# Kernel optimization log

Hardware: AMD Instinct MI355X
Metric: run time of the kernel (lower is better)

Reference implementation:

```python
import jax, jax.numpy as jnp
import numpy as np

B, C, F, H = 262144, 16, 16, 12   # batch, n_clusters, cluster_size, ceil(0.75*F)
HH = 12                           # head hidden = ceil(0.75*C)
EPS = 1e-16


def _linear_init(key, shape, fan_in):
    # torch nn.Linear default: U(-1/sqrt(fan_in), 1/sqrt(fan_in))
    bound = 1.0 / np.sqrt(fan_in)
    return jax.random.uniform(key, shape, jnp.float32, -bound, bound)


def setup_inputs() -> dict:
    key = jax.random.key(0)
    ks = jax.random.split(key, 9)
    x = jax.random.normal(ks[0], (B, C * F), dtype=jnp.float32)
    cluster_idx = jnp.arange(C * F, dtype=jnp.int32).reshape(C, F)
    # Tail autoencoders, stacked over clusters (torch Linear layout [out,in])
    We = _linear_init(ks[1], (C, H, F), F)   # encoder weight per cluster
    be = _linear_init(ks[2], (C, H), F)      # encoder bias
    Wd = _linear_init(ks[3], (C, F, H), H)   # decoder weight per cluster
    bd = _linear_init(ks[4], (C, F), H)      # decoder bias
    # Head autoencoder
    He = _linear_init(ks[5], (HH, C), C)
    hbe = _linear_init(ks[6], (HH,), C)
    Hd = _linear_init(ks[7], (C, HH), HH)
    hbd = _linear_init(ks[8], (C,), HH)
    return {"x": x, "We": We, "be": be, "Wd": Wd, "bd": bd,
            "He": He, "hbe": hbe, "Hd": Hd, "hbd": hbd,
            "cluster_idx": cluster_idx}


def reference(x, We, be, Wd, bd, He, hbe, Hd, hbd, cluster_idx):
    # Gather per-cluster features: [B, C, F]
    xc = x[:, cluster_idx]
    # Normalization with default norm params (min=0, max=1)
    xc = (xc - 0.0) / (1.0 - 0.0 + EPS)
    # Grouped tail autoencoders: sigmoid(Linear) twice, batched over clusters
    h = jax.nn.sigmoid(jnp.einsum('bcf,chf->bch', xc, We) + be)
    rec = jax.nn.sigmoid(jnp.einsum('bch,cfh->bcf', h, Wd) + bd)
    # Per-cluster RMSE over batch and features -> [C]
    loss = jnp.sqrt(jnp.mean((rec - xc) ** 2, axis=(0, 2)))
    loss = jnp.where(loss == 0.0, jnp.float32(0.01), loss)
    # Output normalization (min=0, max=1)
    tails = (loss - 0.0) / (1.0 - 0.0 + EPS)
    # Head autoencoder on the 1-D tail-loss vector
    h2 = jax.nn.sigmoid(He @ tails + hbe)
    head_out = jax.nn.sigmoid(Hd @ h2 + hbd)
    return head_out, tails
```

## Files before the change

### kernel.cpp

```cpp
#include <hip/hip_runtime.h>
#include <math.h>

#define NB      262144
#define NC      16
#define NF      16
#define NH      12
#define NHH     12
#define THREADS 256
#define BX      (NB / THREADS)

__device__ __forceinline__ float sigmoid_fast(float z) {
    float e = __expf(-z);
    return __builtin_amdgcn_rcpf(1.0f + e);
}

__global__ __launch_bounds__(THREADS) void ae_main(
    const float* __restrict__ x,
    const float* __restrict__ We,
    const float* __restrict__ be,
    const float* __restrict__ Wd,
    const float* __restrict__ bd,
    float* __restrict__ partials)
{
    const int tid  = threadIdx.x;
    const int lane = tid & 63;
    const int wave = tid >> 6;
    const size_t b = (size_t)blockIdx.x * THREADS + tid;

    __shared__ float wred[NC][4];

    const float4* xp = reinterpret_cast<const float4*>(x + b * (NC * NF));

    float4 b0 = xp[0], b1 = xp[1], b2 = xp[2], b3 = xp[3];

    #pragma unroll 1
    for (int c = 0; c < NC; ++c) {
        float xc[NF];
        xc[0]=b0.x;  xc[1]=b0.y;  xc[2]=b0.z;  xc[3]=b0.w;
        xc[4]=b1.x;  xc[5]=b1.y;  xc[6]=b1.z;  xc[7]=b1.w;
        xc[8]=b2.x;  xc[9]=b2.y;  xc[10]=b2.z; xc[11]=b2.w;
        xc[12]=b3.x; xc[13]=b3.y; xc[14]=b3.z; xc[15]=b3.w;

        const int cn = (c + 1 < NC) ? (c + 1) : c;
        b0 = xp[4*cn+0]; b1 = xp[4*cn+1]; b2 = xp[4*cn+2]; b3 = xp[4*cn+3];

        const float* wec = We + c * (NH * NF);
        const float* bec = be + c * NH;
        float h[NH];
        #pragma unroll
        for (int hh = 0; hh < NH; ++hh) {
            float z = bec[hh];
            #pragma unroll
            for (int f = 0; f < NF; ++f)
                z = fmaf(xc[f], wec[hh * NF + f], z);
            h[hh] = sigmoid_fast(z);
        }

        const float* wdc = Wd + c * (NF * NH);
        const float* bdc = bd + c * NF;
        float lsum = 0.0f;
        #pragma unroll
        for (int f = 0; f < NF; ++f) {
            float z = bdc[f];
            #pragma unroll
            for (int hh = 0; hh < NH; ++hh)
                z = fmaf(h[hh], wdc[f * NH + hh], z);
            float r = sigmoid_fast(z);
            float d = r - xc[f];
            lsum = fmaf(d, d, lsum);
        }

        #pragma unroll
        for (int off = 32; off > 0; off >>= 1)
            lsum += __shfl_down(lsum, off, 64);
        if (lane == 0) wred[c][wave] = lsum;
    }

    __syncthreads();
    if (tid < NC) {
        float s = wred[tid][0] + wred[tid][1] + wred[tid][2] + wred[tid][3];
        partials[(size_t)blockIdx.x * NC + tid] = s;
    }
}

__global__ __launch_bounds__(1024) void ae_final(
    const float* __restrict__ partials,
    const float* __restrict__ He,
    const float* __restrict__ hbe,
    const float* __restrict__ Hd,
    const float* __restrict__ hbd,
    float* __restrict__ out)
{
    __shared__ float red[NC][65];
    __shared__ float tails_s[NC];
    __shared__ float h2_s[NHH];

    const int tid = threadIdx.x;
    const int c = tid & 15;
    const int g = tid >> 4;

    float s = 0.0f;
    for (int bx = g; bx < BX; bx += 64)
        s += partials[(size_t)bx * NC + c];
    red[c][g] = s;
    __syncthreads();

    if (tid < NC) {
        float t = 0.0f;
        #pragma unroll
        for (int g2 = 0; g2 < 64; ++g2) t += red[tid][g2];
        float loss = sqrtf(t * (1.0f / 4194304.0f));
        if (loss == 0.0f) loss = 0.01f;
        tails_s[tid] = loss;
        out[16 + tid] = loss;
    }
    __syncthreads();

    if (tid < NHH) {
        float z = hbe[tid];
        #pragma unroll
        for (int cc = 0; cc < NC; ++cc)
            z = fmaf(He[tid * NC + cc], tails_s[cc], z);
        h2_s[tid] = 1.0f / (1.0f + __expf(-z));
    }
    __syncthreads();

    if (tid < NC) {
        float z = hbd[tid];
        #pragma unroll
        for (int j = 0; j < NHH; ++j)
            z = fmaf(Hd[tid * NHH + j], h2_s[j], z);
        out[tid] = 1.0f / (1.0f + __expf(-z));
    }
}

extern "C" void kernel_launch(void* const* d_in, const int* in_sizes, int n_in,
                              void* d_out, int out_size, void* d_ws, size_t ws_size,
                              hipStream_t stream) {
    const float* x   = (const float*)d_in[0];
    const float* We  = (const float*)d_in[1];
    const float* be  = (const float*)d_in[2];
    const float* Wd  = (const float*)d_in[3];
    const float* bd  = (const float*)d_in[4];
    const float* He  = (const float*)d_in[5];
    const float* hbe = (const float*)d_in[6];
    const float* Hd  = (const float*)d_in[7];
    const float* hbd = (const float*)d_in[8];

    float* out      = (float*)d_out;
    float* partials = (float*)d_ws;

    ae_main<<<BX, THREADS, 0, stream>>>(x, We, be, Wd, bd, partials);
    ae_final<<<1, 1024, 0, stream>>>(partials, He, hbe, Hd, hbd, out);
}
```

Measured before the change: 452.7 us.

## Split clusters across grid y so each block handles two clusters

The main kernel's grid now has a second dimension over cluster pairs, so each block processes two clusters with all x loads issued up front instead of looping over all 16 with a one-step prefetch. This multiplies the block count by eight to expose more parallelism and memory-level concurrency. The partials layout and the final reduction are reindexed to match. In exchange, each thread's row reads are now strided 128-byte chunks rather than one contiguous 1 KB row, and there are more blocks to schedule.

```diff
diff --git a/kernel.cpp b/kernel.cpp
--- a/kernel.cpp
+++ b/kernel.cpp
@@ -8,6 +8,8 @@
 #define NHH     12
 #define THREADS 256
 #define BX      (NB / THREADS)
+#define NPAIR   8
+#define CPP     2
 
 __device__ __forceinline__ float sigmoid_fast(float z) {
     float e = __expf(-z);
@@ -25,25 +27,28 @@
     const int tid  = threadIdx.x;
     const int lane = tid & 63;
     const int wave = tid >> 6;
+    const int c0   = blockIdx.y * CPP;
     const size_t b = (size_t)blockIdx.x * THREADS + tid;
 
-    __shared__ float wred[NC][4];
+    __shared__ float wred[CPP][4];
 
-    const float4* xp = reinterpret_cast<const float4*>(x + b * (NC * NF));
+    const float4* xp = reinterpret_cast<const float4*>(
+        x + b * (NC * NF) + (size_t)c0 * NF);
 
-    float4 b0 = xp[0], b1 = xp[1], b2 = xp[2], b3 = xp[3];
+    float4 v[2 * 4];
+    #pragma unroll
+    for (int k = 0; k < 8; ++k) v[k] = xp[k];
 
-    #pragma unroll 1
-    for (int c = 0; c < NC; ++c) {
+    #pragma unroll
+    for (int j = 0; j < CPP; ++j) {
         float xc[NF];
-        xc[0]=b0.x;  xc[1]=b0.y;  xc[2]=b0.z;  xc[3]=b0.w;
-        xc[4]=b1.x;  xc[5]=b1.y;  xc[6]=b1.z;  xc[7]=b1.w;
-        xc[8]=b2.x;  xc[9]=b2.y;  xc[10]=b2.z; xc[11]=b2.w;
-        xc[12]=b3.x; xc[13]=b3.y; xc[14]=b3.z; xc[15]=b3.w;
+        #pragma unroll
+        for (int k = 0; k < 4; ++k) {
+            xc[4*k+0] = v[4*j+k].x; xc[4*k+1] = v[4*j+k].y;
+            xc[4*k+2] = v[4*j+k].z; xc[4*k+3] = v[4*j+k].w;
+        }
 
-        const int cn = (c + 1 < NC) ? (c + 1) : c;
-        b0 = xp[4*cn+0]; b1 = xp[4*cn+1]; b2 = xp[4*cn+2]; b3 = xp[4*cn+3];
-
+        const int c = c0 + j;
         const float* wec = We + c * (NH * NF);
         const float* bec = be + c * NH;
         float h[NH];
@@ -73,13 +78,13 @@
         #pragma unroll
         for (int off = 32; off > 0; off >>= 1)
             lsum += __shfl_down(lsum, off, 64);
-        if (lane == 0) wred[c][wave] = lsum;
+        if (lane == 0) wred[j][wave] = lsum;
     }
 
     __syncthreads();
-    if (tid < NC) {
+    if (tid < CPP) {
         float s = wred[tid][0] + wred[tid][1] + wred[tid][2] + wred[tid][3];
-        partials[(size_t)blockIdx.x * NC + tid] = s;
+        partials[((size_t)blockIdx.y * BX + blockIdx.x) * CPP + tid] = s;
     }
 }
 
@@ -98,10 +103,11 @@
     const int tid = threadIdx.x;
     const int c = tid & 15;
     const int g = tid >> 4;
+    const int py = c >> 1, jj = c & 1;
 
     float s = 0.0f;
     for (int bx = g; bx < BX; bx += 64)
-        s += partials[(size_t)bx * NC + c];
+        s += partials[((size_t)py * BX + bx) * CPP + jj];
     red[c][g] = s;
     __syncthreads();
 
@@ -150,6 +156,7 @@
     float* out      = (float*)d_out;
     float* partials = (float*)d_ws;
 
-    ae_main<<<BX, THREADS, 0, stream>>>(x, We, be, Wd, bd, partials);
+    dim3 grid(BX, NPAIR);
+    ae_main<<<grid, THREADS, 0, stream>>>(x, We, be, Wd, bd, partials);
     ae_final<<<1, 1024, 0, stream>>>(partials, He, hbe, Hd, hbd, out);
 }
```

After: 398.6 us. 11.9% less time.
